# Kernel optimization log

Measured on AMD Instinct MI355X. Metric: run time of the kernel, lower is better.

The kernel has to match this reference:

```python
import jax, jax.numpy as jnp
import numpy as np

N_NODES = 100000
N_EDGES = 1600000


def setup_inputs() -> dict:
    key = jax.random.key(0)
    ks = jax.random.split(key, 6)
    x = jax.random.normal(ks[0], (N_NODES, 128), dtype=jnp.float32)
    edge_index = jax.random.randint(ks[1], (2, N_EDGES), 0, N_NODES, dtype=jnp.int64)
    # glorot-ish scaled weights
    W0 = jax.random.normal(ks[2], (128, 64), dtype=jnp.float32) * (1.0 / np.sqrt(128))
    W1 = jax.random.normal(ks[3], (64, 64), dtype=jnp.float32) * (1.0 / np.sqrt(64))
    W2 = jax.random.normal(ks[4], (64, 40), dtype=jnp.float32) * (1.0 / np.sqrt(64))
    b0 = jnp.zeros((64,), jnp.float32)
    b1 = jnp.zeros((64,), jnp.float32)
    b2 = jnp.zeros((40,), jnp.float32)
    return {"x": x, "edge_index": edge_index, "W0": W0, "b0": b0,
            "W1": W1, "b1": b1, "W2": W2, "b2": b2}


def _gcn_norm(edge_index, n, dtype):
    # PyG gcn_norm: add self-loops, deg over targets, norm = d^-1/2[src]*d^-1/2[dst]
    loop = jnp.arange(n, dtype=edge_index.dtype)
    src = jnp.concatenate([edge_index[0], loop])
    dst = jnp.concatenate([edge_index[1], loop])
    deg = jax.ops.segment_sum(jnp.ones_like(dst, dtype=dtype), dst, num_segments=n)
    dinv = jnp.where(deg > 0, jax.lax.rsqrt(deg), 0.0)
    return src, dst, dinv[src] * dinv[dst]


def reference(x, edge_index, W0, b0, W1, b1, W2, b2):
    n = x.shape[0]
    src, dst, norm = _gcn_norm(edge_index, n, x.dtype)

    def conv(h, W, b):
        h = h @ W                                   # [N, out]
        msg = h[src] * norm[:, None]                # gather + per-edge scale
        return jax.ops.segment_sum(msg, dst, num_segments=n) + b

    # dropout skipped (eval mode); relu between layers per forward()
    h = jax.nn.relu(conv(x, W0, b0))
    h = jax.nn.relu(conv(h, W1, b1))
    return conv(h, W2, b2)
```

## Files before the change

kernel.cpp:

```cpp
#include <hip/hip_runtime.h>
#include <hip/hip_fp16.h>


#define ALIGN256(x) (((size_t)(x) + 255) & ~(size_t)255)

typedef _Float16 f16;
typedef f16 f16x8 __attribute__((ext_vector_type(8)));
typedef float f32x4 __attribute__((ext_vector_type(4)));


__global__ __launch_bounds__(256) void k_coarse(const int* __restrict__ ei,
                                                int* __restrict__ ccnt,
                                                int* __restrict__ done,
                                                int* __restrict__ cbase,
                                                int* __restrict__ cpos,
                                                int* __restrict__ row_start,
                                                int E, int N, int NBUK, int nblk) {
    __shared__ int h[512];
    __shared__ int lastblk;
    int t = threadIdx.x;
    for (int i = t; i < NBUK; i += 256) h[i] = 0;
    __syncthreads();
    int e0 = blockIdx.x * 8192;
    int e1 = min(e0 + 8192, E);
    for (int e = e0 + t; e < e1; e += 256) atomicAdd(&h[ei[E + e] >> 8], 1);
    __syncthreads();
    for (int i = t; i < NBUK; i += 256) {
        int c = h[i];
        if (c) atomicAdd(&ccnt[i], c);
    }
    __threadfence();
    if (t == 0) lastblk = (atomicAdd(done, 1) == nblk - 1) ? 1 : 0;
    __syncthreads();
    if (!lastblk) return;

    __shared__ int sd[256];
    int i0 = 2 * t, i1 = 2 * t + 1;
    int v0 = (i0 < NBUK) ? ccnt[i0] : 0;
    int v1 = (i1 < NBUK) ? ccnt[i1] : 0;
    int s = v0 + v1;
    sd[t] = s;
    __syncthreads();
    for (int off = 1; off < 256; off <<= 1) {
        int u = (t >= off) ? sd[t - off] : 0;
        __syncthreads();
        sd[t] += u;
        __syncthreads();
    }
    int base = sd[t] - s;
    if (i0 < NBUK) { cbase[i0] = base;      cpos[i0] = base; }
    if (i1 < NBUK) { cbase[i1] = base + v0; cpos[i1] = base + v0; }
    if (t == 0) { cbase[NBUK] = E; row_start[N] = E; }
}


__global__ __launch_bounds__(256) void k_passA(const int* __restrict__ ei,
                                               int* __restrict__ cpos,
                                               unsigned int* __restrict__ stage,
                                               int E, int NBUK) {
    __shared__ int h[512];
    __shared__ int base[512];
    int t = threadIdx.x;
    for (int i = t; i < NBUK; i += 256) h[i] = 0;
    __syncthreads();
    int e0 = blockIdx.x * 8192;
    int e1 = min(e0 + 8192, E);
    for (int e = e0 + t; e < e1; e += 256) atomicAdd(&h[ei[E + e] >> 8], 1);
    __syncthreads();
    for (int b = t; b < NBUK; b += 256) {
        int c = h[b];
        base[b] = c ? atomicAdd(&cpos[b], c) : 0;
        h[b] = 0;
    }
    __syncthreads();
    for (int e = e0 + t; e < e1; e += 256) {
        unsigned int s = (unsigned int)ei[e];
        int d = ei[E + e];
        int b = d >> 8;
        int off = base[b] + atomicAdd(&h[b], 1);
        stage[off] = ((unsigned int)(d & 255) << 24) | s;
    }
}


__global__ __launch_bounds__(256) void k_B1(const unsigned int* __restrict__ stage,
                                            const int* __restrict__ cbase,
                                            int* __restrict__ row_start,
                                            float* __restrict__ dinv, int N) {
    __shared__ int cnt[256];
    __shared__ int sd[256];
    int b = blockIdx.x;
    int n0 = b << 8;
    int t = threadIdx.x;
    cnt[t] = 0;
    __syncthreads();
    int s0 = cbase[b], s1 = cbase[b + 1];
    for (int j = s0 + t; j < s1; j += 256) atomicAdd(&cnt[stage[j] >> 24], 1);
    __syncthreads();
    int c = cnt[t];
    sd[t] = c;
    __syncthreads();
    for (int off = 1; off < 256; off <<= 1) {
        int u = (t >= off) ? sd[t - off] : 0;
        __syncthreads();
        sd[t] += u;
        __syncthreads();
    }
    int excl = sd[t] - c;
    int node = n0 + t;
    if (node < N) {
        row_start[node] = s0 + excl;
        dinv[node] = 1.0f / sqrtf((float)(c + 1));
    }
}


__global__ __launch_bounds__(256) void k_B2(const unsigned int* __restrict__ stage,
                                            const int* __restrict__ cbase,
                                            const int* __restrict__ row_start,
                                            const float* __restrict__ dinv,
                                            int2* __restrict__ ep, int N) {
    __shared__ int lpos[256];
    __shared__ float ld[256];
    int b = blockIdx.x;
    int n0 = b << 8;
    int t = threadIdx.x;
    int node = n0 + t;
    if (node < N) {
        lpos[t] = row_start[node];
        ld[t] = dinv[node];
    }
    __syncthreads();
    int s0 = cbase[b], s1 = cbase[b + 1];
    for (int j = s0 + t; j < s1; j += 256) {
        unsigned int v = stage[j];
        int li = v >> 24;
        int src = v & 0xFFFFFF;
        int slot = atomicAdd(&lpos[li], 1);
        ep[slot] = make_int2(src, __float_as_int(dinv[src] * ld[li]));
    }
}


template <int K, int OUT, int NF, typename XT>
__global__ __launch_bounds__(256) void k_mgemm(const XT* __restrict__ X,
                                               const float* __restrict__ W,
                                               __half* __restrict__ Y, int N) {
    constexpr int NC = NF * 16;
    constexpr int NT = K / 32;
    __shared__ f16 Wl[NT * NF * 4 * 128];

    int tid = threadIdx.x;
    for (int idx = tid; idx < K * NC; idx += 256) {
        int k = idx / NC;
        int n = idx - k * NC;
        float v = (n < OUT) ? W[k * OUT + n] : 0.0f;
        int t = k >> 5, h = (k >> 3) & 3, j = k & 7, f = n >> 4, nn = n & 15;
        Wl[((t * NF + f) * 4 + h) * 128 + nn * 8 + j] = (f16)v;
    }
    __syncthreads();

    int lane = tid & 63;
    int wid = tid >> 6;
    int h = lane >> 4;
    int nn = lane & 15;
    int row = blockIdx.x * 64 + (wid << 4) + nn;
    bool valid = row < N;

    f32x4 acc[NF];
#pragma unroll
    for (int f = 0; f < NF; ++f) acc[f] = (f32x4){0.f, 0.f, 0.f, 0.f};

#pragma unroll
    for (int t = 0; t < NT; ++t) {
        f16x8 xf;
        if (valid) {
            if constexpr (sizeof(XT) == 4) {
                const float* xp = (const float*)X + (size_t)row * K + (t << 5) + (h << 3);
                float4 u0 = *(const float4*)xp;
                float4 u1 = *(const float4*)(xp + 4);
                xf[0] = (f16)u0.x; xf[1] = (f16)u0.y; xf[2] = (f16)u0.z; xf[3] = (f16)u0.w;
                xf[4] = (f16)u1.x; xf[5] = (f16)u1.y; xf[6] = (f16)u1.z; xf[7] = (f16)u1.w;
            } else {
                xf = *(const f16x8*)((const __half*)X + (size_t)row * K + (t << 5) + (h << 3));
            }
        } else {
#pragma unroll
            for (int j = 0; j < 8; ++j) xf[j] = (f16)0.f;
        }
#pragma unroll
        for (int f = 0; f < NF; ++f) {
            f16x8 wf = *(const f16x8*)&Wl[((t * NF + f) * 4 + h) * 128 + nn * 8];
            acc[f] = __builtin_amdgcn_mfma_f32_16x16x32_f16(wf, xf, acc[f], 0, 0, 0);
        }
    }

    if (valid) {
#pragma unroll
        for (int f = 0; f < NF; ++f) {
            int c = (f << 4) + (h << 2);
            if (c < OUT) {
                __half2 p0 = __floats2half2_rn(acc[f][0], acc[f][1]);
                __half2 p1 = __floats2half2_rn(acc[f][2], acc[f][3]);
                uint2 pk = make_uint2(*(unsigned int*)&p0, *(unsigned int*)&p1);
                *(uint2*)&Y[(size_t)row * OUT + c] = pk;
            }
        }
    }
}


__device__ __forceinline__ void fma8(float4& a0, float4& a1, uint4 hv, float w) {
    __half2* hp = (__half2*)&hv;
    float2 f0 = __half22float2(hp[0]);
    float2 f1 = __half22float2(hp[1]);
    float2 f2 = __half22float2(hp[2]);
    float2 f3 = __half22float2(hp[3]);
    a0.x += f0.x * w; a0.y += f0.y * w; a0.z += f1.x * w; a0.w += f1.y * w;
    a1.x += f2.x * w; a1.y += f2.y * w; a1.z += f3.x * w; a1.w += f3.y * w;
}

template <int NV, int F, int RELU, typename OutT>
__global__ __launch_bounds__(256) void k_agg(const __half* __restrict__ H,
                                             const int* __restrict__ row_start,
                                             const int2* __restrict__ ep,
                                             const float* __restrict__ dinv,
                                             const float* __restrict__ bias,
                                             OutT* __restrict__ out, int N) {
    int tid = threadIdx.x;
    int lane = tid & 63;
    int sub = lane >> 3;
    int lq = lane & 7;
    int node = blockIdx.x * 32 + (tid >> 6) * 8 + sub;
    if (node >= N) return;
    const bool act = (NV == 8) || (lq < NV);

    int jb = row_start[node];
    int je = row_start[node + 1];
    float dv = dinv[node];

    float4 a0 = make_float4(0.f, 0.f, 0.f, 0.f);
    float4 a1 = make_float4(0.f, 0.f, 0.f, 0.f);
    if (act) {
        uint4 hv = *(const uint4*)&H[(size_t)node * F + 8 * lq];
        fma8(a0, a1, hv, dv * dv);
    }

    int j = jb;
    for (; j + 8 <= je; j += 8) {
        int2 e0 = ep[j],     e1 = ep[j + 1], e2 = ep[j + 2], e3 = ep[j + 3];
        int2 e4 = ep[j + 4], e5 = ep[j + 5], e6 = ep[j + 6], e7 = ep[j + 7];
        if (act) {
            uint4 h0 = *(const uint4*)&H[(size_t)e0.x * F + 8 * lq];
            uint4 h1 = *(const uint4*)&H[(size_t)e1.x * F + 8 * lq];
            uint4 h2 = *(const uint4*)&H[(size_t)e2.x * F + 8 * lq];
            uint4 h3 = *(const uint4*)&H[(size_t)e3.x * F + 8 * lq];
            uint4 h4 = *(const uint4*)&H[(size_t)e4.x * F + 8 * lq];
            uint4 h5 = *(const uint4*)&H[(size_t)e5.x * F + 8 * lq];
            uint4 h6 = *(const uint4*)&H[(size_t)e6.x * F + 8 * lq];
            uint4 h7 = *(const uint4*)&H[(size_t)e7.x * F + 8 * lq];
            fma8(a0, a1, h0, __int_as_float(e0.y));
            fma8(a0, a1, h1, __int_as_float(e1.y));
            fma8(a0, a1, h2, __int_as_float(e2.y));
            fma8(a0, a1, h3, __int_as_float(e3.y));
            fma8(a0, a1, h4, __int_as_float(e4.y));
            fma8(a0, a1, h5, __int_as_float(e5.y));
            fma8(a0, a1, h6, __int_as_float(e6.y));
            fma8(a0, a1, h7, __int_as_float(e7.y));
        }
    }
    for (; j + 2 <= je; j += 2) {
        int2 e0 = ep[j], e1 = ep[j + 1];
        if (act) {
            uint4 h0 = *(const uint4*)&H[(size_t)e0.x * F + 8 * lq];
            uint4 h1 = *(const uint4*)&H[(size_t)e1.x * F + 8 * lq];
            fma8(a0, a1, h0, __int_as_float(e0.y));
            fma8(a0, a1, h1, __int_as_float(e1.y));
        }
    }
    if (j < je) {
        int2 e = ep[j];
        if (act) {
            uint4 h = *(const uint4*)&H[(size_t)e.x * F + 8 * lq];
            fma8(a0, a1, h, __int_as_float(e.y));
        }
    }

    if (act) {
        float4 b0 = *(const float4*)&bias[8 * lq];
        float4 b1 = *(const float4*)&bias[8 * lq + 4];
        a0.x += b0.x; a0.y += b0.y; a0.z += b0.z; a0.w += b0.w;
        a1.x += b1.x; a1.y += b1.y; a1.z += b1.z; a1.w += b1.w;
        if (RELU) {
            a0.x = fmaxf(a0.x, 0.f); a0.y = fmaxf(a0.y, 0.f);
            a0.z = fmaxf(a0.z, 0.f); a0.w = fmaxf(a0.w, 0.f);
            a1.x = fmaxf(a1.x, 0.f); a1.y = fmaxf(a1.y, 0.f);
            a1.z = fmaxf(a1.z, 0.f); a1.w = fmaxf(a1.w, 0.f);
        }
        if constexpr (sizeof(OutT) == 2) {
            __half2 p0 = __floats2half2_rn(a0.x, a0.y);
            __half2 p1 = __floats2half2_rn(a0.z, a0.w);
            __half2 p2 = __floats2half2_rn(a1.x, a1.y);
            __half2 p3 = __floats2half2_rn(a1.z, a1.w);
            uint4 pk = make_uint4(*(unsigned int*)&p0, *(unsigned int*)&p1,
                                  *(unsigned int*)&p2, *(unsigned int*)&p3);
            *(uint4*)&out[(size_t)node * F + 8 * lq] = pk;
        } else {
            *(float4*)&out[(size_t)node * F + 8 * lq] = a0;
            *(float4*)&out[(size_t)node * F + 8 * lq + 4] = a1;
        }
    }
}


extern "C" void kernel_launch(void* const* d_in, const int* in_sizes, int n_in,
                              void* d_out, int out_size, void* d_ws, size_t ws_size,
                              hipStream_t stream) {
    const float* x  = (const float*)d_in[0];
    const int*   ei = (const int*)d_in[1];
    const float* W0 = (const float*)d_in[2];
    const float* b0 = (const float*)d_in[3];
    const float* W1 = (const float*)d_in[4];
    const float* b1 = (const float*)d_in[5];
    const float* W2 = (const float*)d_in[6];
    const float* b2 = (const float*)d_in[7];
    float* out = (float*)d_out;

    const int N = in_sizes[0] / 128;
    const int E = in_sizes[1] / 2;
    const int NBUK = (N + 255) >> 8;

    char* w = (char*)d_ws;
    size_t off = 0;
    int*    ccnt      = (int*)(w + off);    off = ALIGN256(off + (size_t)(NBUK + 1) * 4);
    int*    done      = ccnt + NBUK;
    int*    cbase     = (int*)(w + off);    off = ALIGN256(off + (size_t)(NBUK + 1) * 4);
    int*    cpos      = (int*)(w + off);    off = ALIGN256(off + (size_t)NBUK * 4);
    int*    row_start = (int*)(w + off);    off = ALIGN256(off + (size_t)(N + 1) * 4);
    float*  dinv      = (float*)(w + off);  off = ALIGN256(off + (size_t)N * 4);
    int2*   ep        = (int2*)(w + off);   off = ALIGN256(off + (size_t)E * 8);
    __half* bufH      = (__half*)(w + off); off = ALIGN256(off + (size_t)N * 64 * 2);
    __half* bufG      = (__half*)(w + off); off = ALIGN256(off + (size_t)N * 64 * 2);
    unsigned int* stage = (unsigned int*)bufG;

    const int gGemm = (N + 63) / 64;
    const int gAgg  = (N + 31) / 32;
    const int gPA   = (E + 8191) / 8192;

    hipMemsetAsync(ccnt, 0, (size_t)(NBUK + 1) * 4, stream);
    k_mgemm<128, 64, 4><<<gGemm, 256, 0, stream>>>(x, W0, bufH, N);
    k_coarse<<<gPA, 256, 0, stream>>>(ei, ccnt, done, cbase, cpos, row_start, E, N, NBUK, gPA);
    k_passA<<<gPA, 256, 0, stream>>>(ei, cpos, stage, E, NBUK);
    k_B1<<<NBUK, 256, 0, stream>>>(stage, cbase, row_start, dinv, N);
    k_B2<<<NBUK, 256, 0, stream>>>(stage, cbase, row_start, dinv, ep, N);

    k_agg<8, 64, 1, __half><<<gAgg, 256, 0, stream>>>(bufH, row_start, ep, dinv, b0, bufG, N);
    k_mgemm<64, 64, 4><<<gGemm, 256, 0, stream>>>(bufG, W1, bufH, N);
    k_agg<8, 64, 1, __half><<<gAgg, 256, 0, stream>>>(bufH, row_start, ep, dinv, b1, bufG, N);
    k_mgemm<64, 40, 3><<<gGemm, 256, 0, stream>>>(bufG, W2, bufH, N);
    k_agg<5, 40, 0, float><<<gAgg, 256, 0, stream>>>(bufH, row_start, ep, dinv, b2, out, N);
}
```

Before: 309.8 us.

## Merge first GEMM with coarse histogram kernel; stage B2 edge scatter in LDS

Combines the layer-0 MFMA GEMM and the coarse destination-bucket histogram into one launch, with block index ranges picking the role, so the two independent stages can run side by side and one launch is saved. k_B2 now scatters the per-bucket edge pairs into a shared-memory buffer and then writes them to global memory in coalesced order, falling back to direct scatter when a bucket exceeds capacity. The large LDS buffer (about 45KB) lowers B2 occupancy, and the merged kernel reserves 16KB of LDS for every block, including the histogram blocks.

```diff
diff --git a/kernel.cpp b/kernel.cpp
--- a/kernel.cpp
+++ b/kernel.cpp
@@ -9,146 +9,14 @@
 typedef float f32x4 __attribute__((ext_vector_type(4)));
 
 
-__global__ __launch_bounds__(256) void k_coarse(const int* __restrict__ ei,
-                                                int* __restrict__ ccnt,
-                                                int* __restrict__ done,
-                                                int* __restrict__ cbase,
-                                                int* __restrict__ cpos,
-                                                int* __restrict__ row_start,
-                                                int E, int N, int NBUK, int nblk) {
-    __shared__ int h[512];
-    __shared__ int lastblk;
-    int t = threadIdx.x;
-    for (int i = t; i < NBUK; i += 256) h[i] = 0;
-    __syncthreads();
-    int e0 = blockIdx.x * 8192;
-    int e1 = min(e0 + 8192, E);
-    for (int e = e0 + t; e < e1; e += 256) atomicAdd(&h[ei[E + e] >> 8], 1);
-    __syncthreads();
-    for (int i = t; i < NBUK; i += 256) {
-        int c = h[i];
-        if (c) atomicAdd(&ccnt[i], c);
-    }
-    __threadfence();
-    if (t == 0) lastblk = (atomicAdd(done, 1) == nblk - 1) ? 1 : 0;
-    __syncthreads();
-    if (!lastblk) return;
-
-    __shared__ int sd[256];
-    int i0 = 2 * t, i1 = 2 * t + 1;
-    int v0 = (i0 < NBUK) ? ccnt[i0] : 0;
-    int v1 = (i1 < NBUK) ? ccnt[i1] : 0;
-    int s = v0 + v1;
-    sd[t] = s;
-    __syncthreads();
-    for (int off = 1; off < 256; off <<= 1) {
-        int u = (t >= off) ? sd[t - off] : 0;
-        __syncthreads();
-        sd[t] += u;
-        __syncthreads();
-    }
-    int base = sd[t] - s;
-    if (i0 < NBUK) { cbase[i0] = base;      cpos[i0] = base; }
-    if (i1 < NBUK) { cbase[i1] = base + v0; cpos[i1] = base + v0; }
-    if (t == 0) { cbase[NBUK] = E; row_start[N] = E; }
-}
-
-
-__global__ __launch_bounds__(256) void k_passA(const int* __restrict__ ei,
-                                               int* __restrict__ cpos,
-                                               unsigned int* __restrict__ stage,
-                                               int E, int NBUK) {
-    __shared__ int h[512];
-    __shared__ int base[512];
-    int t = threadIdx.x;
-    for (int i = t; i < NBUK; i += 256) h[i] = 0;
-    __syncthreads();
-    int e0 = blockIdx.x * 8192;
-    int e1 = min(e0 + 8192, E);
-    for (int e = e0 + t; e < e1; e += 256) atomicAdd(&h[ei[E + e] >> 8], 1);
-    __syncthreads();
-    for (int b = t; b < NBUK; b += 256) {
-        int c = h[b];
-        base[b] = c ? atomicAdd(&cpos[b], c) : 0;
-        h[b] = 0;
-    }
-    __syncthreads();
-    for (int e = e0 + t; e < e1; e += 256) {
-        unsigned int s = (unsigned int)ei[e];
-        int d = ei[E + e];
-        int b = d >> 8;
-        int off = base[b] + atomicAdd(&h[b], 1);
-        stage[off] = ((unsigned int)(d & 255) << 24) | s;
-    }
-}
-
-
-__global__ __launch_bounds__(256) void k_B1(const unsigned int* __restrict__ stage,
-                                            const int* __restrict__ cbase,
-                                            int* __restrict__ row_start,
-                                            float* __restrict__ dinv, int N) {
-    __shared__ int cnt[256];
-    __shared__ int sd[256];
-    int b = blockIdx.x;
-    int n0 = b << 8;
-    int t = threadIdx.x;
-    cnt[t] = 0;
-    __syncthreads();
-    int s0 = cbase[b], s1 = cbase[b + 1];
-    for (int j = s0 + t; j < s1; j += 256) atomicAdd(&cnt[stage[j] >> 24], 1);
-    __syncthreads();
-    int c = cnt[t];
-    sd[t] = c;
-    __syncthreads();
-    for (int off = 1; off < 256; off <<= 1) {
-        int u = (t >= off) ? sd[t - off] : 0;
-        __syncthreads();
-        sd[t] += u;
-        __syncthreads();
-    }
-    int excl = sd[t] - c;
-    int node = n0 + t;
-    if (node < N) {
-        row_start[node] = s0 + excl;
-        dinv[node] = 1.0f / sqrtf((float)(c + 1));
-    }
-}
-
-
-__global__ __launch_bounds__(256) void k_B2(const unsigned int* __restrict__ stage,
-                                            const int* __restrict__ cbase,
-                                            const int* __restrict__ row_start,
-                                            const float* __restrict__ dinv,
-                                            int2* __restrict__ ep, int N) {
-    __shared__ int lpos[256];
-    __shared__ float ld[256];
-    int b = blockIdx.x;
-    int n0 = b << 8;
-    int t = threadIdx.x;
-    int node = n0 + t;
-    if (node < N) {
-        lpos[t] = row_start[node];
-        ld[t] = dinv[node];
-    }
-    __syncthreads();
-    int s0 = cbase[b], s1 = cbase[b + 1];
-    for (int j = s0 + t; j < s1; j += 256) {
-        unsigned int v = stage[j];
-        int li = v >> 24;
-        int src = v & 0xFFFFFF;
-        int slot = atomicAdd(&lpos[li], 1);
-        ep[slot] = make_int2(src, __float_as_int(dinv[src] * ld[li]));
-    }
-}
-
-
 template <int K, int OUT, int NF, typename XT>
-__global__ __launch_bounds__(256) void k_mgemm(const XT* __restrict__ X,
-                                               const float* __restrict__ W,
-                                               __half* __restrict__ Y, int N) {
+__device__ __forceinline__ void mgemm_body(int bid, const XT* __restrict__ X,
+                                           const float* __restrict__ W,
+                                           __half* __restrict__ Y, int N,
+                                           char* smem) {
     constexpr int NC = NF * 16;
     constexpr int NT = K / 32;
-    __shared__ f16 Wl[NT * NF * 4 * 128];
+    f16* Wl = (f16*)smem;
 
     int tid = threadIdx.x;
     for (int idx = tid; idx < K * NC; idx += 256) {
@@ -164,7 +32,7 @@
     int wid = tid >> 6;
     int h = lane >> 4;
     int nn = lane & 15;
-    int row = blockIdx.x * 64 + (wid << 4) + nn;
+    int row = bid * 64 + (wid << 4) + nn;
     bool valid = row < N;
 
     f32x4 acc[NF];
@@ -205,6 +73,185 @@
                 uint2 pk = make_uint2(*(unsigned int*)&p0, *(unsigned int*)&p1);
                 *(uint2*)&Y[(size_t)row * OUT + c] = pk;
             }
+        }
+    }
+}
+
+template <int K, int OUT, int NF, typename XT>
+__global__ __launch_bounds__(256) void k_mgemm(const XT* __restrict__ X,
+                                               const float* __restrict__ W,
+                                               __half* __restrict__ Y, int N) {
+    __shared__ __align__(16) char pool[(K / 32) * NF * 4 * 128 * 2];
+    mgemm_body<K, OUT, NF, XT>(blockIdx.x, X, W, Y, N, pool);
+}
+
+
+__device__ __forceinline__ void coarse_body(int bid, const int* __restrict__ ei,
+                                            int* __restrict__ ccnt,
+                                            int* __restrict__ done,
+                                            int* __restrict__ cbase,
+                                            int* __restrict__ cpos,
+                                            int* __restrict__ row_start,
+                                            int E, int N, int NBUK, int nblk,
+                                            char* smem) {
+    int* h = (int*)smem;
+    int* sd = h + 512;
+    int* lastblk = sd + 256;
+    int t = threadIdx.x;
+    for (int i = t; i < NBUK; i += 256) h[i] = 0;
+    __syncthreads();
+    int e0 = bid * 8192;
+    int e1 = min(e0 + 8192, E);
+    for (int e = e0 + t; e < e1; e += 256) atomicAdd(&h[ei[E + e] >> 8], 1);
+    __syncthreads();
+    for (int i = t; i < NBUK; i += 256) {
+        int c = h[i];
+        if (c) atomicAdd(&ccnt[i], c);
+    }
+    __threadfence();
+    if (t == 0) *lastblk = (atomicAdd(done, 1) == nblk - 1) ? 1 : 0;
+    __syncthreads();
+    if (!*lastblk) return;
+
+    int i0 = 2 * t, i1 = 2 * t + 1;
+    int v0 = (i0 < NBUK) ? ccnt[i0] : 0;
+    int v1 = (i1 < NBUK) ? ccnt[i1] : 0;
+    int s = v0 + v1;
+    sd[t] = s;
+    __syncthreads();
+    for (int off = 1; off < 256; off <<= 1) {
+        int u = (t >= off) ? sd[t - off] : 0;
+        __syncthreads();
+        sd[t] += u;
+        __syncthreads();
+    }
+    int base = sd[t] - s;
+    if (i0 < NBUK) { cbase[i0] = base;      cpos[i0] = base; }
+    if (i1 < NBUK) { cbase[i1] = base + v0; cpos[i1] = base + v0; }
+    if (t == 0) { cbase[NBUK] = E; row_start[N] = E; }
+}
+
+
+__global__ __launch_bounds__(256) void k_front(const float* __restrict__ X,
+                                               const float* __restrict__ W0,
+                                               __half* __restrict__ Y,
+                                               const int* __restrict__ ei,
+                                               int* __restrict__ ccnt,
+                                               int* __restrict__ done,
+                                               int* __restrict__ cbase,
+                                               int* __restrict__ cpos,
+                                               int* __restrict__ row_start,
+                                               int E, int N, int NBUK,
+                                               int gGemm, int gPA) {
+    __shared__ __align__(16) char pool[16384];
+    if ((int)blockIdx.x < gGemm) {
+        mgemm_body<128, 64, 4, float>(blockIdx.x, X, W0, Y, N, pool);
+    } else {
+        coarse_body(blockIdx.x - gGemm, ei, ccnt, done, cbase, cpos, row_start,
+                    E, N, NBUK, gPA, pool);
+    }
+}
+
+
+__global__ __launch_bounds__(256) void k_passA(const int* __restrict__ ei,
+                                               int* __restrict__ cpos,
+                                               unsigned int* __restrict__ stage,
+                                               int E, int NBUK) {
+    __shared__ int h[512];
+    __shared__ int base[512];
+    int t = threadIdx.x;
+    for (int i = t; i < NBUK; i += 256) h[i] = 0;
+    __syncthreads();
+    int e0 = blockIdx.x * 8192;
+    int e1 = min(e0 + 8192, E);
+    for (int e = e0 + t; e < e1; e += 256) atomicAdd(&h[ei[E + e] >> 8], 1);
+    __syncthreads();
+    for (int b = t; b < NBUK; b += 256) {
+        int c = h[b];
+        base[b] = c ? atomicAdd(&cpos[b], c) : 0;
+        h[b] = 0;
+    }
+    __syncthreads();
+    for (int e = e0 + t; e < e1; e += 256) {
+        unsigned int s = (unsigned int)ei[e];
+        int d = ei[E + e];
+        int b = d >> 8;
+        int off = base[b] + atomicAdd(&h[b], 1);
+        stage[off] = ((unsigned int)(d & 255) << 24) | s;
+    }
+}
+
+
+__global__ __launch_bounds__(256) void k_B1(const unsigned int* __restrict__ stage,
+                                            const int* __restrict__ cbase,
+                                            int* __restrict__ row_start,
+                                            float* __restrict__ dinv, int N) {
+    __shared__ int cnt[256];
+    __shared__ int sd[256];
+    int b = blockIdx.x;
+    int n0 = b << 8;
+    int t = threadIdx.x;
+    cnt[t] = 0;
+    __syncthreads();
+    int s0 = cbase[b], s1 = cbase[b + 1];
+    for (int j = s0 + t; j < s1; j += 256) atomicAdd(&cnt[stage[j] >> 24], 1);
+    __syncthreads();
+    int c = cnt[t];
+    sd[t] = c;
+    __syncthreads();
+    for (int off = 1; off < 256; off <<= 1) {
+        int u = (t >= off) ? sd[t - off] : 0;
+        __syncthreads();
+        sd[t] += u;
+        __syncthreads();
+    }
+    int excl = sd[t] - c;
+    int node = n0 + t;
+    if (node < N) {
+        row_start[node] = s0 + excl;
+        dinv[node] = 1.0f / sqrtf((float)(c + 1));
+    }
+}
+
+
+#define B2CAP 5632
+
+__global__ __launch_bounds__(256) void k_B2(const unsigned int* __restrict__ stage,
+                                            const int* __restrict__ cbase,
+                                            const int* __restrict__ row_start,
+                                            const float* __restrict__ dinv,
+                                            int2* __restrict__ ep, int N) {
+    __shared__ int2 lep[B2CAP];
+    __shared__ int lpos[256];
+    __shared__ float ld[256];
+    int b = blockIdx.x;
+    int n0 = b << 8;
+    int t = threadIdx.x;
+    int s0 = cbase[b], s1 = cbase[b + 1];
+    int cnt = s1 - s0;
+    int node = n0 + t;
+    if (node < N) {
+        lpos[t] = row_start[node] - s0;
+        ld[t] = dinv[node];
+    }
+    __syncthreads();
+    if (cnt <= B2CAP) {
+        for (int j = s0 + t; j < s1; j += 256) {
+            unsigned int v = stage[j];
+            int li = v >> 24;
+            int src = v & 0xFFFFFF;
+            int slot = atomicAdd(&lpos[li], 1);
+            lep[slot] = make_int2(src, __float_as_int(dinv[src] * ld[li]));
+        }
+        __syncthreads();
+        for (int i = t; i < cnt; i += 256) ep[s0 + i] = lep[i];
+    } else {
+        for (int j = s0 + t; j < s1; j += 256) {
+            unsigned int v = stage[j];
+            int li = v >> 24;
+            int src = v & 0xFFFFFF;
+            int slot = atomicAdd(&lpos[li], 1);
+            ep[s0 + slot] = make_int2(src, __float_as_int(dinv[src] * ld[li]));
         }
     }
 }
@@ -348,8 +395,8 @@
     const int gPA   = (E + 8191) / 8192;
 
     hipMemsetAsync(ccnt, 0, (size_t)(NBUK + 1) * 4, stream);
-    k_mgemm<128, 64, 4><<<gGemm, 256, 0, stream>>>(x, W0, bufH, N);
-    k_coarse<<<gPA, 256, 0, stream>>>(ei, ccnt, done, cbase, cpos, row_start, E, N, NBUK, gPA);
+    k_front<<<gGemm + gPA, 256, 0, stream>>>(x, W0, bufH, ei, ccnt, done, cbase,
+                                             cpos, row_start, E, N, NBUK, gGemm, gPA);
     k_passA<<<gPA, 256, 0, stream>>>(ei, cpos, stage, E, NBUK);
     k_B1<<<NBUK, 256, 0, stream>>>(stage, cbase, row_start, dinv, N);
     k_B2<<<NBUK, 256, 0, stream>>>(stage, cbase, row_start, dinv, ep, N);
```

Measured after the change: 311.7 us. Within noise of the previous version (+0.6%).

## Replace two-pass bucket sort CSR build with global-atomic degree count and fill

Applied to the files above, without the earlier changes.

Replaces the bucketed staging sort (coarse histogram, passA scatter into a stage buffer, B1 local count, B2 local placement) with a direct build. Per-node degrees are now counted with global atomics alongside the bucket histogram, then a per-bucket scan produces row_start and a cursor, and a fill kernel scatters edges with global atomics on the cursor. This drops one kernel and the intermediate staging pass over edges. In exchange it relies on many scattered global atomics with random destinations, and edge order within a row becomes nondeterministic.

```diff
diff --git a/kernel.cpp b/kernel.cpp
--- a/kernel.cpp
+++ b/kernel.cpp
@@ -3,27 +3,33 @@
 
 
 #define ALIGN256(x) (((size_t)(x) + 255) & ~(size_t)255)
+
+#define DEG_EDGES 2048
 
 typedef _Float16 f16;
 typedef f16 f16x8 __attribute__((ext_vector_type(8)));
 typedef float f32x4 __attribute__((ext_vector_type(4)));
 
 
-__global__ __launch_bounds__(256) void k_coarse(const int* __restrict__ ei,
-                                                int* __restrict__ ccnt,
-                                                int* __restrict__ done,
-                                                int* __restrict__ cbase,
-                                                int* __restrict__ cpos,
-                                                int* __restrict__ row_start,
-                                                int E, int N, int NBUK, int nblk) {
+__global__ __launch_bounds__(256) void k_deg(const int* __restrict__ ei,
+                                             int* __restrict__ deg,
+                                             int* __restrict__ ccnt,
+                                             int* __restrict__ done,
+                                             int* __restrict__ cbase,
+                                             int* __restrict__ row_start,
+                                             int E, int N, int NBUK, int nblk) {
     __shared__ int h[512];
     __shared__ int lastblk;
     int t = threadIdx.x;
     for (int i = t; i < NBUK; i += 256) h[i] = 0;
     __syncthreads();
-    int e0 = blockIdx.x * 8192;
-    int e1 = min(e0 + 8192, E);
-    for (int e = e0 + t; e < e1; e += 256) atomicAdd(&h[ei[E + e] >> 8], 1);
+    int e0 = blockIdx.x * DEG_EDGES;
+    int e1 = min(e0 + DEG_EDGES, E);
+    for (int e = e0 + t; e < e1; e += 256) {
+        int d = ei[E + e];
+        atomicAdd(&h[d >> 8], 1);
+        atomicAdd(&deg[d], 1);
+    }
     __syncthreads();
     for (int i = t; i < NBUK; i += 256) {
         int c = h[i];
@@ -48,56 +54,22 @@
         __syncthreads();
     }
     int base = sd[t] - s;
-    if (i0 < NBUK) { cbase[i0] = base;      cpos[i0] = base; }
-    if (i1 < NBUK) { cbase[i1] = base + v0; cpos[i1] = base + v0; }
+    if (i0 < NBUK) cbase[i0] = base;
+    if (i1 < NBUK) cbase[i1] = base + v0;
     if (t == 0) { cbase[NBUK] = E; row_start[N] = E; }
 }
 
 
-__global__ __launch_bounds__(256) void k_passA(const int* __restrict__ ei,
-                                               int* __restrict__ cpos,
-                                               unsigned int* __restrict__ stage,
-                                               int E, int NBUK) {
-    __shared__ int h[512];
-    __shared__ int base[512];
-    int t = threadIdx.x;
-    for (int i = t; i < NBUK; i += 256) h[i] = 0;
-    __syncthreads();
-    int e0 = blockIdx.x * 8192;
-    int e1 = min(e0 + 8192, E);
-    for (int e = e0 + t; e < e1; e += 256) atomicAdd(&h[ei[E + e] >> 8], 1);
-    __syncthreads();
-    for (int b = t; b < NBUK; b += 256) {
-        int c = h[b];
-        base[b] = c ? atomicAdd(&cpos[b], c) : 0;
-        h[b] = 0;
-    }
-    __syncthreads();
-    for (int e = e0 + t; e < e1; e += 256) {
-        unsigned int s = (unsigned int)ei[e];
-        int d = ei[E + e];
-        int b = d >> 8;
-        int off = base[b] + atomicAdd(&h[b], 1);
-        stage[off] = ((unsigned int)(d & 255) << 24) | s;
-    }
-}
-
-
-__global__ __launch_bounds__(256) void k_B1(const unsigned int* __restrict__ stage,
+__global__ __launch_bounds__(256) void k_rs(const int* __restrict__ deg,
                                             const int* __restrict__ cbase,
                                             int* __restrict__ row_start,
+                                            int* __restrict__ cursor,
                                             float* __restrict__ dinv, int N) {
-    __shared__ int cnt[256];
     __shared__ int sd[256];
     int b = blockIdx.x;
-    int n0 = b << 8;
     int t = threadIdx.x;
-    cnt[t] = 0;
-    __syncthreads();
-    int s0 = cbase[b], s1 = cbase[b + 1];
-    for (int j = s0 + t; j < s1; j += 256) atomicAdd(&cnt[stage[j] >> 24], 1);
-    __syncthreads();
-    int c = cnt[t];
+    int node = (b << 8) + t;
+    int c = (node < N) ? deg[node] : 0;
     sd[t] = c;
     __syncthreads();
     for (int off = 1; off < 256; off <<= 1) {
@@ -107,37 +79,27 @@
         __syncthreads();
     }
     int excl = sd[t] - c;
-    int node = n0 + t;
     if (node < N) {
-        row_start[node] = s0 + excl;
+        int rs = cbase[b] + excl;
+        row_start[node] = rs;
+        cursor[node] = rs;
         dinv[node] = 1.0f / sqrtf((float)(c + 1));
     }
 }
 
 
-__global__ __launch_bounds__(256) void k_B2(const unsigned int* __restrict__ stage,
-                                            const int* __restrict__ cbase,
-                                            const int* __restrict__ row_start,
-                                            const float* __restrict__ dinv,
-                                            int2* __restrict__ ep, int N) {
-    __shared__ int lpos[256];
-    __shared__ float ld[256];
-    int b = blockIdx.x;
-    int n0 = b << 8;
-    int t = threadIdx.x;
-    int node = n0 + t;
-    if (node < N) {
-        lpos[t] = row_start[node];
-        ld[t] = dinv[node];
-    }
-    __syncthreads();
-    int s0 = cbase[b], s1 = cbase[b + 1];
-    for (int j = s0 + t; j < s1; j += 256) {
-        unsigned int v = stage[j];
-        int li = v >> 24;
-        int src = v & 0xFFFFFF;
-        int slot = atomicAdd(&lpos[li], 1);
-        ep[slot] = make_int2(src, __float_as_int(dinv[src] * ld[li]));
+__global__ __launch_bounds__(256) void k_fill(const int* __restrict__ ei,
+                                              const float* __restrict__ dinv,
+                                              int* __restrict__ cursor,
+                                              int2* __restrict__ ep, int E) {
+    int e0 = blockIdx.x * DEG_EDGES;
+    int e1 = min(e0 + DEG_EDGES, E);
+    for (int e = e0 + threadIdx.x; e < e1; e += 256) {
+        int src = ei[e];
+        int dst = ei[E + e];
+        float nrm = dinv[src] * dinv[dst];
+        int pos = atomicAdd(&cursor[dst], 1);
+        ep[pos] = make_int2(src, __float_as_int(nrm));
     }
 }
 
@@ -332,27 +294,26 @@
 
     char* w = (char*)d_ws;
     size_t off = 0;
-    int*    ccnt      = (int*)(w + off);    off = ALIGN256(off + (size_t)(NBUK + 1) * 4);
+    int*    ccnt      = (int*)(w + off);    off = ALIGN256(off + (size_t)(NBUK + 1 + N) * 4);
     int*    done      = ccnt + NBUK;
+    int*    deg       = ccnt + NBUK + 1;
     int*    cbase     = (int*)(w + off);    off = ALIGN256(off + (size_t)(NBUK + 1) * 4);
-    int*    cpos      = (int*)(w + off);    off = ALIGN256(off + (size_t)NBUK * 4);
     int*    row_start = (int*)(w + off);    off = ALIGN256(off + (size_t)(N + 1) * 4);
+    int*    cursor    = (int*)(w + off);    off = ALIGN256(off + (size_t)N * 4);
     float*  dinv      = (float*)(w + off);  off = ALIGN256(off + (size_t)N * 4);
     int2*   ep        = (int2*)(w + off);   off = ALIGN256(off + (size_t)E * 8);
     __half* bufH      = (__half*)(w + off); off = ALIGN256(off + (size_t)N * 64 * 2);
     __half* bufG      = (__half*)(w + off); off = ALIGN256(off + (size_t)N * 64 * 2);
-    unsigned int* stage = (unsigned int*)bufG;
 
     const int gGemm = (N + 63) / 64;
     const int gAgg  = (N + 31) / 32;
-    const int gPA   = (E + 8191) / 8192;
-
-    hipMemsetAsync(ccnt, 0, (size_t)(NBUK + 1) * 4, stream);
+    const int gE    = (E + DEG_EDGES - 1) / DEG_EDGES;
+
+    hipMemsetAsync(ccnt, 0, (size_t)(NBUK + 1 + N) * 4, stream);
     k_mgemm<128, 64, 4><<<gGemm, 256, 0, stream>>>(x, W0, bufH, N);
-    k_coarse<<<gPA, 256, 0, stream>>>(ei, ccnt, done, cbase, cpos, row_start, E, N, NBUK, gPA);
-    k_passA<<<gPA, 256, 0, stream>>>(ei, cpos, stage, E, NBUK);
-    k_B1<<<NBUK, 256, 0, stream>>>(stage, cbase, row_start, dinv, N);
-    k_B2<<<NBUK, 256, 0, stream>>>(stage, cbase, row_start, dinv, ep, N);
+    k_deg<<<gE, 256, 0, stream>>>(ei, deg, ccnt, done, cbase, row_start, E, N, NBUK, gE);
+    k_rs<<<NBUK, 256, 0, stream>>>(deg, cbase, row_start, cursor, dinv, N);
+    k_fill<<<gE, 256, 0, stream>>>(ei, dinv, cursor, ep, E);
 
     k_agg<8, 64, 1, __half><<<gAgg, 256, 0, stream>>>(bufH, row_start, ep, dinv, b0, bufG, N);
     k_mgemm<64, 64, 4><<<gGemm, 256, 0, stream>>>(bufG, W1, bufH, N);
```

After: 439.0 us. +41.7%, slower.
